# Optimization experiments

Measured on AMD Instinct MI355X. Metric: run time of the kernel, lower is better.

Reference implementation:

```python
import jax, jax.numpy as jnp
import numpy as np

B, N, DIN, H, DOUT = 32, 1024, 256, 256, 256
NEG = 9000000000000000.0  # -9e15 masking trick from the original code


def setup_inputs() -> dict:
    key = jax.random.key(0)
    ks = jax.random.split(key, 10)
    x = jax.random.normal(ks[0], (B, N, DIN), dtype=jnp.float32)
    # binary float mask (1 = edge present)
    mask = jax.random.randint(ks[1], (B, N, N), 0, 2).astype(jnp.float32)
    s = 0.02
    Wv = jax.random.normal(ks[2], (DIN, H), dtype=jnp.float32) * s
    bv = jnp.zeros((H,), jnp.float32)
    Wk = jax.random.normal(ks[3], (DIN, H), dtype=jnp.float32) * s
    bk = jnp.zeros((H,), jnp.float32)
    Wq = jax.random.normal(ks[4], (DIN, H), dtype=jnp.float32) * s
    bq = jnp.zeros((H,), jnp.float32)
    Wo = jax.random.normal(ks[5], (H, DOUT), dtype=jnp.float32) * s
    bo = jnp.zeros((DOUT,), jnp.float32)
    return {"x": x, "mask": mask, "Wv": Wv, "bv": bv, "Wk": Wk, "bk": bk,
            "Wq": Wq, "bq": bq, "Wo": Wo, "bo": bo}


def reference(x, mask, Wv, bv, Wk, bk, Wq, bq, Wo, bo):
    # x: [B,N,din], mask: [B,N,N]
    v = jax.nn.relu(x @ Wv + bv)              # [B,N,H]
    q = jax.nn.relu(x @ Wq + bq)              # [B,N,H]
    k = jax.nn.relu(x @ Wk + bk)              # [B,N,H]
    scores = jnp.einsum('bnh,bmh->bnm', q, k)  # QK^T, [B,N,N]
    att = jax.nn.softmax(scores * mask - NEG * (1.0 - mask), axis=-1)
    out = jnp.einsum('bnm,bmh->bnh', att, v)   # AV
    return jax.nn.relu(out @ Wo + bo)          # [B,N,d_out]
```

## Files before the change

### kernel.cpp

```cpp
#include <hip/hip_runtime.h>


typedef __attribute__((ext_vector_type(4))) float    f32x4;
typedef __attribute__((ext_vector_type(8))) short    s16x8;
typedef __attribute__((ext_vector_type(4))) short    s16x4;
typedef unsigned long long u64;

__device__ __forceinline__ short f2b(float f) {
    union { float f; unsigned u; } v; v.f = f;
    unsigned r = v.u + 0x7FFFu + ((v.u >> 16) & 1u);
    return (short)(r >> 16);
}

__device__ __forceinline__ void gl_lds16(const short* g, short* l) {
    __builtin_amdgcn_global_load_lds(
        (const __attribute__((address_space(1))) unsigned int*)g,
        (__attribute__((address_space(3))) unsigned int*)l, 16, 0, 0);
}

__global__ void prep_w(const float* __restrict__ Wq, const float* __restrict__ Wk,
                       const float* __restrict__ Wv, const float* __restrict__ Wo,
                       short* __restrict__ Wt) {
    int idx = blockIdx.x * 256 + threadIdx.x;
    int w = idx >> 16, rem = idx & 65535;
    int n = rem >> 8, kk = rem & 255;
    const float* W = (w == 0) ? Wq : (w == 1) ? Wk : (w == 2) ? Wv : Wo;
    Wt[idx] = f2b(W[kk * 256 + n]);
}

__global__ __launch_bounds__(256) void qkv_gemm(
        const float* __restrict__ x, const short* __restrict__ Wt,
        const float* __restrict__ bq, const float* __restrict__ bk, const float* __restrict__ bv,
        short* __restrict__ qO, short* __restrict__ kO, short* __restrict__ vtO) {
    __shared__ short a_lds[128][72];
    __shared__ short b_lds[3][64][72];
    const int tid = threadIdx.x;
    const int bm = blockIdx.x >> 2, bn = blockIdx.x & 3;
    const int s0 = bm * 128, n0 = bn * 64;
    const int wid = tid >> 6, l = tid & 63, lo4 = l & 15, hi4 = l >> 4;
    const int wm = wid >> 1, wn = wid & 1;

    f32x4 acc[3][4][2];
    #pragma unroll
    for (int w = 0; w < 3; ++w)
        #pragma unroll
        for (int mi = 0; mi < 4; ++mi)
            #pragma unroll
            for (int ni = 0; ni < 2; ++ni)
                acc[w][mi][ni] = (f32x4){0.f, 0.f, 0.f, 0.f};

    for (int kt = 0; kt < 4; ++kt) {
        const int k0 = kt * 64;
        #pragma unroll
        for (int i = 0; i < 8; ++i) {
            int ch = i * 256 + tid;
            int row = ch >> 4, c4 = (ch & 15) * 4;
            f32x4 xv = *(const f32x4*)(x + (size_t)(s0 + row) * 256 + k0 + c4);
            s16x4 pk = { f2b(xv.x), f2b(xv.y), f2b(xv.z), f2b(xv.w) };
            *(s16x4*)&a_lds[row][c4] = pk;
        }
        #pragma unroll
        for (int w = 0; w < 3; ++w) {
            #pragma unroll
            for (int i = 0; i < 2; ++i) {
                int ch = i * 256 + tid;
                int n = ch >> 3, c8 = (ch & 7) * 8;
                *(s16x8*)&b_lds[w][n][c8] =
                    *(const s16x8*)(Wt + (size_t)w * 65536 + (size_t)(n0 + n) * 256 + k0 + c8);
            }
        }
        __syncthreads();
        s16x8 af[4][2];
        #pragma unroll
        for (int mi = 0; mi < 4; ++mi)
            #pragma unroll
            for (int kk = 0; kk < 2; ++kk)
                af[mi][kk] = *(s16x8*)&a_lds[wm * 64 + mi * 16 + lo4][kk * 32 + hi4 * 8];
        #pragma unroll
        for (int w = 0; w < 3; ++w)
            #pragma unroll
            for (int ni = 0; ni < 2; ++ni)
                #pragma unroll
                for (int kk = 0; kk < 2; ++kk) {
                    s16x8 bfr = *(s16x8*)&b_lds[w][wn * 32 + ni * 16 + lo4][kk * 32 + hi4 * 8];
                    #pragma unroll
                    for (int mi = 0; mi < 4; ++mi)
                        acc[w][mi][ni] = __builtin_amdgcn_mfma_f32_16x16x32_bf16(
                            af[mi][kk], bfr, acc[w][mi][ni], 0, 0, 0);
                }
        __syncthreads();
    }

    const float* bias[3] = { bq, bk, bv };
    for (int w = 0; w < 3; ++w) {
        #pragma unroll
        for (int mi = 0; mi < 4; ++mi)
            #pragma unroll
            for (int ni = 0; ni < 2; ++ni)
                #pragma unroll
                for (int j = 0; j < 4; ++j) {
                    int r = wm * 64 + mi * 16 + hi4 * 4 + j;
                    int c = wn * 32 + ni * 16 + lo4;
                    float v = acc[w][mi][ni][j] + bias[w][n0 + c];
                    a_lds[r][c] = f2b(fmaxf(v, 0.f));
                }
        __syncthreads();
        if (w == 0) {
            #pragma unroll
            for (int i = 0; i < 4; ++i) {
                int ch = i * 256 + tid;
                int row = ch >> 3, c8 = (ch & 7) * 8;
                *(s16x8*)(qO + (size_t)(s0 + row) * 256 + n0 + c8) = *(s16x8*)&a_lds[row][c8];
            }
        } else if (w == 1) {
            #pragma unroll
            for (int i = 0; i < 4; ++i) {
                int ch = i * 256 + tid;
                int row = ch >> 3, c8 = (ch & 7) * 8;
                int swz = ((c8 >> 3) ^ (row & 7)) * 8;
                *(s16x8*)(kO + (size_t)(s0 + row) * 256 + n0 + swz) = *(s16x8*)&a_lds[row][c8];
            }
        } else {
            int bb = s0 >> 10, nn = s0 & 1023;
            #pragma unroll
            for (int i = 0; i < 4; ++i) {
                int ch = i * 256 + tid;
                int h = ch >> 4, sc = (ch & 15) * 8;
                s16x8 t;
                #pragma unroll
                for (int e = 0; e < 8; ++e) t[e] = a_lds[sc + e][h];
                int cil = sc >> 3;
                int swz = (cil & 8) | ((cil & 7) ^ ((n0 + h) & 7));
                *(s16x8*)(vtO + ((size_t)bb * 256 + n0 + h) * 1024 + nn + swz * 8) = t;
            }
        }
        __syncthreads();
    }
}

__global__ __launch_bounds__(768) void attn(
        const short* __restrict__ q, const short* __restrict__ k,
        const short* __restrict__ vt, const float* __restrict__ mask,
        short* __restrict__ attv) {
    __shared__ short kbuf[2][16384];
    __shared__ short vbuf[2][16384];
    __shared__ short p_lds[8][16][72];
    __shared__ u64 B_lds[2][32][4];
    const int tid = threadIdx.x, wid = tid >> 6, l = tid & 63;
    const int lo4 = l & 15, hi4 = l >> 4;
    const int bid = blockIdx.x;
    const int swz = (bid & 7) * 32 + (bid >> 3);
    const int b = swz >> 3, qb = swz & 7;
    const size_t bq0 = (size_t)b * 1024 + qb * 128;

    if (wid >= 8) {
        const int pw = wid - 8;
        const float* mb = mask + (bq0 + pw * 32 + (l >> 4)) * 1024 + (l & 15) * 4;
#define PACK(bufi, c0_) do {                                                   \
        f32x4 va_[8];                                                          \
        _Pragma("unroll") for (int i_ = 0; i_ < 8; ++i_)                       \
            va_[i_] = *(const f32x4*)(mb + (size_t)i_ * 4096 + (c0_));         \
        _Pragma("unroll") for (int i_ = 0; i_ < 8; ++i_) {                     \
            u64 b0_ = __ballot(va_[i_].x != 0.f);                              \
            u64 b1_ = __ballot(va_[i_].y != 0.f);                              \
            u64 b2_ = __ballot(va_[i_].z != 0.f);                              \
            u64 b3_ = __ballot(va_[i_].w != 0.f);                              \
            if (l < 4) {                                                       \
                u64 w_ = (l == 0) ? b0_ : (l == 1) ? b1_ : (l == 2) ? b2_ : b3_; \
                B_lds[bufi][pw * 8 + i_][l] = w_;                              \
            } } } while (0)
        PACK(0, 0);
        for (int t = 0; t < 16; ++t) {
            if (t < 15) PACK((t + 1) & 1, (t + 1) * 64);
            asm volatile("s_waitcnt lgkmcnt(0)" ::: "memory");
            __builtin_amdgcn_s_barrier();
            __builtin_amdgcn_s_barrier();
        }
#undef PACK
        return;
    }

    const int q0 = qb * 128 + wid * 16;
    const size_t bq_row = (size_t)b * 1024 + q0;
    const short* kb  = k  + (size_t)b * 1024 * 256;
    const short* vtg = vt + (size_t)b * 256 * 1024;

#define STAGE_K(bufi, c0_) do { const short* sg_ = kb + (size_t)(c0_) * 256;          \
    _Pragma("unroll") for (int i_ = 0; i_ < 4; ++i_) { int cb_ = i_ * 512 + wid * 64; \
        gl_lds16(sg_ + (size_t)(cb_ + l) * 8, &kbuf[bufi][cb_ * 8]); } } while (0)
#define STAGE_V(bufi, c0_) do {                                                       \
    _Pragma("unroll") for (int i_ = 0; i_ < 4; ++i_) { int cb_ = i_ * 512 + wid * 64; \
        int ch_ = cb_ + l; int h_ = ch_ >> 3, cc_ = ch_ & 7;                          \
        gl_lds16(vtg + (size_t)h_ * 1024 + (c0_) + cc_ * 8, &vbuf[bufi][cb_ * 8]); } } while (0)

    s16x8 qf[8];
    {
        const short* qp = q + (bq_row + lo4) * 256 + hi4 * 8;
        #pragma unroll
        for (int t = 0; t < 8; ++t) qf[t] = *(const s16x8*)(qp + t * 32);
    }
    STAGE_K(0, 0);
    STAGE_V(0, 0);

    f32x4 oacc[16];
    #pragma unroll
    for (int t = 0; t < 16; ++t) oacc[t] = (f32x4){0.f, 0.f, 0.f, 0.f};
    float m_run[4] = { -1e30f, -1e30f, -1e30f, -1e30f };
    float l_run[4] = { 0.f, 0.f, 0.f, 0.f };

    for (int t = 0; t < 16; ++t) {
        const int cur = t & 1;
        const int c0 = t * 64;
        if (t < 15) {
            STAGE_K(cur ^ 1, c0 + 64);
            asm volatile("s_waitcnt vmcnt(8)" ::: "memory");
        } else {
            asm volatile("s_waitcnt vmcnt(4)" ::: "memory");
        }
        __builtin_amdgcn_s_barrier();
        f32x4 s[4];
        #pragma unroll
        for (int ct = 0; ct < 4; ++ct) s[ct] = (f32x4){0.f, 0.f, 0.f, 0.f};
        __builtin_amdgcn_s_setprio(1);
        #pragma unroll
        for (int ct = 0; ct < 4; ++ct) {
            int row = ct * 16 + lo4, rx = row & 7;
            #pragma unroll
            for (int tt = 0; tt < 8; ++tt) {
                int ch = tt * 4 + hi4;
                int sc = (ch & 24) | ((ch & 7) ^ rx);
                s16x8 kf = *(s16x8*)&kbuf[cur][row * 256 + sc * 8];
                s[ct] = __builtin_amdgcn_mfma_f32_16x16x32_bf16(qf[tt], kf, s[ct], 0, 0, 0);
            }
        }
        __builtin_amdgcn_s_setprio(0);
        u64 mk = B_lds[t & 1][wid * 4 + hi4][lo4 & 3];
        const unsigned sh0 = (unsigned)(lo4 >> 2);
        float sm[4][4];
        #pragma unroll
        for (int j = 0; j < 4; ++j) {
            unsigned wsx = (unsigned)(mk >> (j * 16 + sh0));
            sm[0][j] = (wsx & 1u)    ? s[0][j] : -1e30f;
            sm[1][j] = (wsx & 16u)   ? s[1][j] : -1e30f;
            sm[2][j] = (wsx & 256u)  ? s[2][j] : -1e30f;
            sm[3][j] = (wsx & 4096u) ? s[3][j] : -1e30f;
        }
        float scale[4], p[4][4];
        #pragma unroll
        for (int j = 0; j < 4; ++j) {
            float tmx = fmaxf(fmaxf(sm[0][j], sm[1][j]), fmaxf(sm[2][j], sm[3][j]));
            tmx = fmaxf(tmx, __shfl_xor(tmx, 1));
            tmx = fmaxf(tmx, __shfl_xor(tmx, 2));
            tmx = fmaxf(tmx, __shfl_xor(tmx, 4));
            tmx = fmaxf(tmx, __shfl_xor(tmx, 8));
            float mnew = fmaxf(m_run[j], tmx);
            scale[j] = __expf(m_run[j] - mnew);
            m_run[j] = mnew;
            float su = 0.f;
            #pragma unroll
            for (int ct = 0; ct < 4; ++ct) { p[ct][j] = __expf(sm[ct][j] - mnew); su += p[ct][j]; }
            su += __shfl_xor(su, 1);
            su += __shfl_xor(su, 2);
            su += __shfl_xor(su, 4);
            su += __shfl_xor(su, 8);
            l_run[j] = l_run[j] * scale[j] + su;
        }
        #pragma unroll
        for (int tt = 0; tt < 16; ++tt)
            #pragma unroll
            for (int j = 0; j < 4; ++j) oacc[tt][j] *= scale[j];
        #pragma unroll
        for (int ct = 0; ct < 4; ++ct)
            #pragma unroll
            for (int j = 0; j < 4; ++j)
                p_lds[wid][hi4 * 4 + j][ct * 16 + lo4] = f2b(p[ct][j]);
        asm volatile("s_waitcnt lgkmcnt(0)" ::: "memory");
        __builtin_amdgcn_sched_barrier(0);
        s16x8 pa0 = *(s16x8*)&p_lds[wid][lo4][hi4 * 8];
        s16x8 pa1 = *(s16x8*)&p_lds[wid][lo4][32 + hi4 * 8];
        if (t < 15) {
            STAGE_V(cur ^ 1, c0 + 64);
            asm volatile("s_waitcnt vmcnt(8)" ::: "memory");
        } else {
            asm volatile("s_waitcnt vmcnt(0)" ::: "memory");
        }
        __builtin_amdgcn_s_barrier();
        __builtin_amdgcn_s_setprio(1);
        #pragma unroll
        for (int nt = 0; nt < 16; ++nt) {
            int h = nt * 16 + lo4, hx = h & 7;
            s16x8 vf0 = *(s16x8*)&vbuf[cur][h * 64 + (hi4 ^ hx) * 8];
            s16x8 vf1 = *(s16x8*)&vbuf[cur][h * 64 + ((hi4 + 4) ^ hx) * 8];
            oacc[nt] = __builtin_amdgcn_mfma_f32_16x16x32_bf16(pa0, vf0, oacc[nt], 0, 0, 0);
            oacc[nt] = __builtin_amdgcn_mfma_f32_16x16x32_bf16(pa1, vf1, oacc[nt], 0, 0, 0);
        }
        __builtin_amdgcn_s_setprio(0);
    }
    float inv[4];
    #pragma unroll
    for (int j = 0; j < 4; ++j) inv[j] = 1.f / l_run[j];
    #pragma unroll
    for (int g = 0; g < 4; ++g) {
        asm volatile("s_waitcnt lgkmcnt(0)" ::: "memory");
        #pragma unroll
        for (int ntl = 0; ntl < 4; ++ntl)
            #pragma unroll
            for (int j = 0; j < 4; ++j)
                p_lds[wid][hi4 * 4 + j][ntl * 16 + lo4] = f2b(oacc[g * 4 + ntl][j] * inv[j]);
        asm volatile("s_waitcnt lgkmcnt(0)" ::: "memory");
        __builtin_amdgcn_sched_barrier(0);
        s16x8 r0 = *(s16x8*)&p_lds[wid][lo4][hi4 * 16];
        s16x8 r1 = *(s16x8*)&p_lds[wid][lo4][hi4 * 16 + 8];
        short* op = attv + (bq_row + lo4) * 256 + g * 64 + hi4 * 16;
        *(s16x8*)op = r0;
        *(s16x8*)(op + 8) = r1;
    }
#undef STAGE_K
#undef STAGE_V
}

__global__ __launch_bounds__(256) void out_gemm(
        const short* __restrict__ a, const short* __restrict__ Wto,
        const float* __restrict__ bo, float* __restrict__ out) {
    __shared__ short a_lds[128][72];
    __shared__ short b_lds[64][72];
    __shared__ float bounce[128][68];
    const int tid = threadIdx.x;
    const int bm = blockIdx.x >> 2, bn = blockIdx.x & 3;
    const int s0 = bm * 128, n0 = bn * 64;
    const int wid = tid >> 6, l = tid & 63, lo4 = l & 15, hi4 = l >> 4;
    const int wm = wid >> 1, wn = wid & 1;
    f32x4 acc[4][2];
    #pragma unroll
    for (int mi = 0; mi < 4; ++mi)
        #pragma unroll
        for (int ni = 0; ni < 2; ++ni) acc[mi][ni] = (f32x4){0.f, 0.f, 0.f, 0.f};

    for (int kt = 0; kt < 4; ++kt) {
        const int k0 = kt * 64;
        #pragma unroll
        for (int i = 0; i < 4; ++i) {
            int ch = i * 256 + tid;
            int row = ch >> 3, c8 = (ch & 7) * 8;
            *(s16x8*)&a_lds[row][c8] = *(const s16x8*)(a + (size_t)(s0 + row) * 256 + k0 + c8);
        }
        #pragma unroll
        for (int i = 0; i < 2; ++i) {
            int ch = i * 256 + tid;
            int n = ch >> 3, c8 = (ch & 7) * 8;
            *(s16x8*)&b_lds[n][c8] = *(const s16x8*)(Wto + (size_t)(n0 + n) * 256 + k0 + c8);
        }
        __syncthreads();
        s16x8 af[4][2];
        #pragma unroll
        for (int mi = 0; mi < 4; ++mi)
            #pragma unroll
            for (int kk = 0; kk < 2; ++kk)
                af[mi][kk] = *(s16x8*)&a_lds[wm * 64 + mi * 16 + lo4][kk * 32 + hi4 * 8];
        #pragma unroll
        for (int ni = 0; ni < 2; ++ni)
            #pragma unroll
            for (int kk = 0; kk < 2; ++kk) {
                s16x8 bfr = *(s16x8*)&b_lds[wn * 32 + ni * 16 + lo4][kk * 32 + hi4 * 8];
                #pragma unroll
                for (int mi = 0; mi < 4; ++mi)
                    acc[mi][ni] = __builtin_amdgcn_mfma_f32_16x16x32_bf16(
                        af[mi][kk], bfr, acc[mi][ni], 0, 0, 0);
            }
        __syncthreads();
    }
    #pragma unroll
    for (int mi = 0; mi < 4; ++mi)
        #pragma unroll
        for (int ni = 0; ni < 2; ++ni)
            #pragma unroll
            for (int j = 0; j < 4; ++j) {
                int r = wm * 64 + mi * 16 + hi4 * 4 + j;
                int c = wn * 32 + ni * 16 + lo4;
                bounce[r][c] = fmaxf(acc[mi][ni][j] + bo[n0 + c], 0.f);
            }
    __syncthreads();
    #pragma unroll
    for (int i = 0; i < 8; ++i) {
        int ch = i * 256 + tid;
        int row = ch >> 4, c4 = (ch & 15) * 4;
        *(f32x4*)(out + (size_t)(s0 + row) * 256 + n0 + c4) = *(f32x4*)&bounce[row][c4];
    }
}

extern "C" void kernel_launch(void* const* d_in, const int* in_sizes, int n_in,
                              void* d_out, int out_size, void* d_ws, size_t ws_size,
                              hipStream_t stream) {
    const float* x    = (const float*)d_in[0];
    const float* mask = (const float*)d_in[1];
    const float* Wv   = (const float*)d_in[2];
    const float* bv   = (const float*)d_in[3];
    const float* Wk   = (const float*)d_in[4];
    const float* bk   = (const float*)d_in[5];
    const float* Wq   = (const float*)d_in[6];
    const float* bq   = (const float*)d_in[7];
    const float* Wo   = (const float*)d_in[8];
    const float* bo   = (const float*)d_in[9];
    float* out = (float*)d_out;

    char* ws = (char*)d_ws;
    short* Wt   = (short*)ws;
    short* qB   = (short*)(ws + (1 << 20));
    short* kB   = qB  + (size_t)32768 * 256;
    short* vtB  = kB  + (size_t)32768 * 256;
    short* avB  = vtB + (size_t)32768 * 256;
    (void)in_sizes; (void)n_in; (void)out_size; (void)ws_size;

    prep_w<<<1024, 256, 0, stream>>>(Wq, Wk, Wv, Wo, Wt);
    qkv_gemm<<<1024, 256, 0, stream>>>(x, Wt, bq, bk, bv, qB, kB, vtB);
    attn<<<256, 768, 0, stream>>>(qB, kB, vtB, mask, avB);
    out_gemm<<<1024, 256, 0, stream>>>(avB, Wt + 3 * 65536, bo, out);
}
```

Measured before the change: 147.9 us.

## Deepen mask-packing pipeline to two tiles ahead with four-slot bitmask buffer

The producer waves that turn the float mask into ballot bitmasks now prefetch mask tiles two iterations ahead. Global loads are issued between the two per-iteration barriers, and the ballots and LDS writes happen after the second barrier. The bitmask buffer in shared memory grows from two to four slots, and the consumer indexes it with t&3. The goal is to hide global-load latency of the mask stream behind the attention compute. The cost is more shared memory and a more involved barrier protocol.

```diff
diff --git a/kernel.cpp b/kernel.cpp
--- a/kernel.cpp
+++ b/kernel.cpp
@@ -145,7 +145,7 @@
     __shared__ short kbuf[2][16384];
     __shared__ short vbuf[2][16384];
     __shared__ short p_lds[8][16][72];
-    __shared__ u64 B_lds[2][32][4];
+    __shared__ u64 B_lds[4][32][4];
     const int tid = threadIdx.x, wid = tid >> 6, l = tid & 63;
     const int lo4 = l & 15, hi4 = l >> 4;
     const int bid = blockIdx.x;
@@ -156,27 +156,37 @@
     if (wid >= 8) {
         const int pw = wid - 8;
         const float* mb = mask + (bq0 + pw * 32 + (l >> 4)) * 1024 + (l & 15) * 4;
-#define PACK(bufi, c0_) do {                                                   \
-        f32x4 va_[8];                                                          \
-        _Pragma("unroll") for (int i_ = 0; i_ < 8; ++i_)                       \
-            va_[i_] = *(const f32x4*)(mb + (size_t)i_ * 4096 + (c0_));         \
-        _Pragma("unroll") for (int i_ = 0; i_ < 8; ++i_) {                     \
-            u64 b0_ = __ballot(va_[i_].x != 0.f);                              \
-            u64 b1_ = __ballot(va_[i_].y != 0.f);                              \
-            u64 b2_ = __ballot(va_[i_].z != 0.f);                              \
-            u64 b3_ = __ballot(va_[i_].w != 0.f);                              \
+        f32x4 va[4], vb[4];
+#define PISSUE(BUF, tau, g) do {                                               \
+        _Pragma("unroll") for (int i_ = 0; i_ < 4; ++i_)                       \
+            BUF[i_] = *(const f32x4*)(mb + (size_t)((g) * 16 + i_ * 4) * 1024  \
+                                         + (size_t)(tau) * 64); } while (0)
+#define PBALLOT(BUF, tau, g) do {                                              \
+        _Pragma("unroll") for (int i_ = 0; i_ < 4; ++i_) {                     \
+            u64 b0_ = __ballot(BUF[i_].x != 0.f);                              \
+            u64 b1_ = __ballot(BUF[i_].y != 0.f);                              \
+            u64 b2_ = __ballot(BUF[i_].z != 0.f);                              \
+            u64 b3_ = __ballot(BUF[i_].w != 0.f);                              \
             if (l < 4) {                                                       \
                 u64 w_ = (l == 0) ? b0_ : (l == 1) ? b1_ : (l == 2) ? b2_ : b3_; \
-                B_lds[bufi][pw * 8 + i_][l] = w_;                              \
+                B_lds[(tau) & 3][pw * 8 + (g) * 4 + i_][l] = w_;               \
             } } } while (0)
-        PACK(0, 0);
+        PISSUE(va, 0, 0); PISSUE(vb, 0, 1);
+        PBALLOT(va, 0, 0); PBALLOT(vb, 0, 1);
+        PISSUE(va, 1, 0); PISSUE(vb, 1, 1);
+        PBALLOT(va, 1, 0); PBALLOT(vb, 1, 1);
+        asm volatile("s_waitcnt lgkmcnt(0)" ::: "memory");
         for (int t = 0; t < 16; ++t) {
-            if (t < 15) PACK((t + 1) & 1, (t + 1) * 64);
-            asm volatile("s_waitcnt lgkmcnt(0)" ::: "memory");
             __builtin_amdgcn_s_barrier();
+            if (t < 14) { PISSUE(va, t + 2, 0); PISSUE(vb, t + 2, 1); }
             __builtin_amdgcn_s_barrier();
-        }
-#undef PACK
+            if (t < 14) {
+                PBALLOT(va, t + 2, 0); PBALLOT(vb, t + 2, 1);
+                asm volatile("s_waitcnt lgkmcnt(0)" ::: "memory");
+            }
+        }
+#undef PISSUE
+#undef PBALLOT
         return;
     }
 
@@ -234,7 +244,7 @@
             }
         }
         __builtin_amdgcn_s_setprio(0);
-        u64 mk = B_lds[t & 1][wid * 4 + hi4][lo4 & 3];
+        u64 mk = B_lds[t & 3][wid * 4 + hi4][lo4 & 3];
         const unsigned sh0 = (unsigned)(lo4 >> 2);
         float sm[4][4];
         #pragma unroll
```

Result: faster. 141.7 us (-4.1%).
